# Kernel tuning notes

Measured on AMD Instinct MI355X. Metric: run time of the kernel, lower is better.

Reference implementation:

```python
import jax, jax.numpy as jnp
import numpy as np

B, C, U, LEN, K = 32, 16, 16, 128, 4  # batch, channels, units, image side, cheb order
POWERS = K + 1


def _path_chebyshev(n, k):
    """Chebyshev polynomials T_0..T_k of the rescaled normalized Laplacian of an
    undirected path graph with n nodes. Returns [k+1, n, n] float32."""
    A = np.zeros((n, n), dtype=np.float64)
    A[np.arange(n - 1), np.arange(1, n)] = 1.0
    A = A + A.T
    d = A.sum(axis=1)
    dinv = 1.0 / np.sqrt(d)
    L = np.eye(n) - dinv[:, None] * A * dinv[None, :]   # normalized Laplacian
    Lt = L - np.eye(n)                                   # rescaled: 2L/lambda_max - I, lambda_max=2
    T = [np.eye(n), Lt]
    for _ in range(2, k + 1):
        T.append(2.0 * Lt @ T[-1] - T[-2])
    return np.stack(T[: k + 1]).astype(np.float32)


def setup_inputs() -> dict:
    key = jax.random.key(0)
    kx, kc = jax.random.split(key)
    x = jax.random.normal(kx, (B, C, LEN, LEN), dtype=jnp.float32)
    coefs = 0.001 * jax.random.normal(kc, (POWERS, POWERS, C, U), dtype=jnp.float32)
    cheb = jnp.asarray(_path_chebyshev(LEN, K))  # same graph for both axes
    return {"x": x, "coefs": coefs, "cheb1": cheb, "cheb2": cheb}


def reference(x, coefs, cheb1, cheb2):
    # out[b,u,p,q] = sum_{k1,k2,c,h,w} coefs[k1,k2,c,u] * cheb1[k1,h,p] * x[b,c,h,w] * cheb2[k2,w,q]
    t1 = jnp.einsum('bchw,khp->bkcpw', x, cheb1)        # apply cheb1 along H
    s = jnp.einsum('bkcpw,klcu->blupw', t1, coefs)      # contract k1 and channels
    out = jnp.einsum('blupw,lwq->bupq', s, cheb2)       # apply cheb2 along W, contract k2
    return out
```

## Files before the change

kernel.cpp:

```cpp
#include <hip/hip_runtime.h>
#include <hip/hip_bf16.h>

#define LEN 128
#define NB 32
#define NC 16
#define NU 16
#define NK 5
#define KC 80
#define KCP 96

typedef unsigned int uint32;
typedef unsigned short ushort16;
typedef __attribute__((ext_vector_type(8))) short bf16x8;
typedef __attribute__((ext_vector_type(4))) float f32x4;

#define MFMA(a, b, c) __builtin_amdgcn_mfma_f32_16x16x32_bf16(a, b, c, 0, 0, 0)

#define SIG(r) (((r) & 15) ^ (((r) >> 3) & 15))

static __device__ inline ushort16 f2bf(float f) {
    union { float f; uint32 u; } v; v.f = f;
    uint32 u = v.u;
    uint32 r = (u + 0x7fffu + ((u >> 16) & 1u)) >> 16;
    return (ushort16)r;
}
static __device__ inline uint32 pkbf(float a, float b) {
    return (uint32)f2bf(a) | ((uint32)f2bf(b) << 16);
}
static __device__ inline bf16x8 frag16(const void* p) {
    return *(const bf16x8*)p;
}

__global__ __launch_bounds__(256) void kprep(const float* __restrict__ x,
                                             const float* __restrict__ coefs,
                                             const float* __restrict__ cheb1,
                                             const float* __restrict__ cheb2,
                                             ushort16* __restrict__ xF,
                                             ushort16* __restrict__ cheb1F,
                                             ushort16* __restrict__ cheb2F,
                                             ushort16* __restrict__ coefF,
                                             ushort16* __restrict__ t1, int ident) {
    __shared__ __align__(16) uint32 Xs[128 * 64];
    const int blk = blockIdx.x, tid = threadIdx.x;
    if (blk < 512) {
        const int bc = blk;
        const float* xp = x + (size_t)bc * (LEN * LEN);
        {
            int w = tid & 127, hg = tid >> 7;
            #pragma unroll
            for (int uu = 0; uu < 8; ++uu) {
                int u = hg * 8 + uu;
                uint4 d;
                uint32* dp = (uint32*)&d;
                #pragma unroll
                for (int t = 0; t < 4; ++t) {
                    int h2 = u * 4 + t;
                    dp[t] = pkbf(xp[(2 * h2) * LEN + w], xp[(2 * h2 + 1) * LEN + w]);
                }
                *(uint4*)(Xs + w * 64 + ((u ^ SIG(w)) << 2)) = d;
            }
        }
        if (ident) {
            const int b = bc >> 4, c = bc & 15;
            int p = tid >> 1, half = tid & 1;
            const float4* src = (const float4*)(xp + p * LEN + half * 64);
            ushort16* dst = t1 + ((size_t)(b * LEN + p) * KC + c) * LEN + half * 64;
            #pragma unroll
            for (int i = 0; i < 16; ++i) {
                float4 v = src[i];
                uint2 d;
                d.x = pkbf(v.x, v.y);
                d.y = pkbf(v.z, v.w);
                *(uint2*)(dst + i * 4) = d;
            }
        }
        __syncthreads();
        ushort16* dst = xF + (size_t)bc * 16384;
        #pragma unroll
        for (int i = 0; i < 8; ++i) {
            int n = tid + i * 256;
            int lane = n & 63, fk = n >> 6;
            int wrow = (fk >> 2) * 16 + (lane & 15);
            int u = (fk & 3) * 4 + (lane >> 4);
            uint4 v = *(const uint4*)(Xs + wrow * 64 + ((u ^ SIG(wrow)) << 2));
            *(uint4*)(dst + (size_t)n * 8) = v;
        }
    } else {
        int i = (blk - 512) * 256 + tid;
        if (i < 81920) {
            int j = i & 7, lane = (i >> 3) & 63, ks = (i >> 9) & 3, nt = i >> 11;
            int kp = nt * 16 + (lane & 15);
            int k = kp >> 7, p = kp & 127;
            int h = ks * 32 + ((lane >> 4) << 3) + j;
            cheb1F[i] = f2bf(cheb1[(k * LEN + h) * LEN + p]);
        } else if (i < 163840) {
            int i2 = i - 81920;
            int j = i2 & 7, lane = (i2 >> 3) & 63, t = i2 >> 9;
            int ks = t % 20, nt = t / 20;
            int q = nt * 16 + (lane & 15);
            int lw = ks * 32 + ((lane >> 4) << 3) + j;
            int l = lw >> 7, w = lw & 127;
            cheb2F[i2] = f2bf(cheb2[(l * LEN + w) * LEN + q]);
        } else {
            int i3 = i - 163840;
            int j = i3 & 7, lane = (i3 >> 3) & 63, t = i3 >> 9;
            int ks = t % 3, nt = t / 3;
            int lu = nt * 16 + (lane & 15);
            int l = lu >> 4, u = lu & 15;
            int kc = ks * 32 + ((lane >> 4) << 3) + j;
            int k = kc >> 4, c = kc & 15;
            coefF[i3] = (kc < KC) ? f2bf(coefs[((k * NK + l) * NC + c) * NU + u]) : (ushort16)0;
        }
    }
}

__global__ __launch_bounds__(256, 5) void k1_mfma(const ushort16* __restrict__ xF,
                                                  const ushort16* __restrict__ cheb1F,
                                                  const float* __restrict__ x,
                                                  ushort16* __restrict__ t1, int b0, int ident) {
    __shared__ __align__(16) uint32 Bs[64 * 64];
    const int c = blockIdx.x, bl = blockIdx.y, z = blockIdx.z;
    const int b = b0 + bl;
    const int tid = threadIdx.x;
    const int lane = tid & 63, wm = tid >> 6;
    const int m16 = lane & 15, g = lane >> 4;

    if (!ident && z == 0) {
        const float* xp = x + (size_t)(b * NC + c) * (LEN * LEN);
        int p = tid >> 1, half = tid & 1;
        const float4* src = (const float4*)(xp + p * LEN + half * 64);
        ushort16* dst = t1 + ((size_t)(bl * LEN + p) * KC + c) * LEN + half * 64;
        #pragma unroll
        for (int i = 0; i < 16; ++i) {
            float4 v = src[i];
            uint2 d;
            d.x = pkbf(v.x, v.y);
            d.y = pkbf(v.z, v.w);
            *(uint2*)(dst + i * 4) = d;
        }
    }

    const ushort16* xFb = xF + ((size_t)(b * NC + c)) * 16384;

    f32x4 acc[2][4];
    #pragma unroll
    for (int mi = 0; mi < 2; ++mi)
        #pragma unroll
        for (int ni = 0; ni < 4; ++ni) acc[mi][ni] = (f32x4)0.f;

    #pragma unroll
    for (int ks = 0; ks < 4; ++ks) {
        bf16x8 Af[2], Bf[4];
        #pragma unroll
        for (int mi = 0; mi < 2; ++mi) {
            int mt = wm * 2 + mi;
            Af[mi] = frag16(xFb + ((size_t)(mt * 4 + ks) * 64 + lane) * 8);
        }
        #pragma unroll
        for (int ni = 0; ni < 4; ++ni) {
            int nt = 8 + z * 4 + ni;
            Bf[ni] = frag16(cheb1F + ((size_t)(nt * 4 + ks) * 64 + lane) * 8);
        }
        #pragma unroll
        for (int mi = 0; mi < 2; ++mi)
            #pragma unroll
            for (int ni = 0; ni < 4; ++ni)
                acc[mi][ni] = MFMA(Af[mi], Bf[ni], acc[mi][ni]);
    }

    #pragma unroll
    for (int ni = 0; ni < 4; ++ni)
        #pragma unroll
        for (int mi = 0; mi < 2; ++mi) {
            int rr = ni * 16 + m16;
            int wu = wm * 32 + mi * 16 + g * 4;
            uint2 d;
            d.x = pkbf(acc[mi][ni][0], acc[mi][ni][1]);
            d.y = pkbf(acc[mi][ni][2], acc[mi][ni][3]);
            int u = wu >> 3;
            *(uint2*)(Bs + rr * 64 + ((u ^ SIG(rr)) << 2) + ((wu >> 1) & 3)) = d;
        }
    __syncthreads();

    #pragma unroll
    for (int i = 0; i < 4; ++i) {
        int n = tid + i * 256;
        int rr = n >> 4, wsg = n & 15;
        uint4 v = *(const uint4*)(Bs + rr * 64 + ((wsg ^ SIG(rr)) << 2));
        int kp = 128 + z * 64 + rr;
        int k = kp >> 7, p = kp & 127;
        *(uint4*)(t1 + ((size_t)((bl * LEN + p) * KC + k * NC + c)) * LEN + wsg * 8) = v;
    }
}

__global__ __launch_bounds__(256, 5) void k2_mfma(const ushort16* __restrict__ t1,
                                                  const ushort16* __restrict__ coefF,
                                                  const ushort16* __restrict__ cheb2F,
                                                  float* __restrict__ out, int b0) {
    __shared__ __align__(16) uint32 sm[128 * 64];
    const int p = blockIdx.x, bl = blockIdx.y, b = b0 + bl;
    const int tid = threadIdx.x;
    const int lane = tid & 63, wave = tid >> 6;
    const int n16 = lane & 15, g = lane >> 4;

    const uint32* t1u = (const uint32*)(t1 + (size_t)(bl * LEN + p) * (KC * LEN));
    uint4 Av[3], Bv[3];
    #pragma unroll
    for (int i = 0; i < 3; ++i) {
        int it = tid + i * 256;
        if (it < 640) {
            int a2 = it >> 4, wq = it & 15;
            const uint32* src = t1u + a2 * 128 + wq * 4;
            Av[i] = *(const uint4*)(src);
            Bv[i] = *(const uint4*)(src + 64);
        }
    }
    #pragma unroll
    for (int i = 0; i < 4; ++i) {
        int idx = tid + i * 256;
        int row = idx >> 3, d = idx & 7;
        int u = 10 + (d >> 2);
        sm[row * 64 + ((u ^ SIG(row)) << 2) + (d & 3)] = 0;
    }
    #pragma unroll
    for (int i = 0; i < 3; ++i) {
        int it = tid + i * 256;
        if (it < 640) {
            int a2 = it >> 4, wq = it & 15;
            const uint32* av = (const uint32*)&Av[i];
            const uint32* bv = (const uint32*)&Bv[i];
            int u = a2 >> 2, lo = a2 & 3;
            #pragma unroll
            for (int j = 0; j < 4; ++j) {
                int r0 = wq * 8 + 2 * j, r1 = r0 + 1;
                sm[r0 * 64 + ((u ^ SIG(r0)) << 2) + lo] = (av[j] & 0xffffu) | (bv[j] << 16);
                sm[r1 * 64 + ((u ^ SIG(r1)) << 2) + lo] = (av[j] >> 16) | (bv[j] & 0xffff0000u);
            }
        }
    }
    __syncthreads();

    f32x4 acc[2][5];
    #pragma unroll
    for (int mi = 0; mi < 2; ++mi)
        #pragma unroll
        for (int ni = 0; ni < 5; ++ni) acc[mi][ni] = (f32x4)0.f;

    #pragma unroll
    for (int ks = 0; ks < 3; ++ks) {
        bf16x8 Af[2], Bf[5];
        #pragma unroll
        for (int mi = 0; mi < 2; ++mi) {
            int row = wave * 32 + mi * 16 + n16;
            Af[mi] = frag16(sm + row * 64 + (((ks * 4 + g) ^ SIG(row)) << 2));
        }
        #pragma unroll
        for (int ni = 0; ni < 5; ++ni)
            Bf[ni] = frag16(coefF + ((size_t)(ni * 3 + ks) * 64 + lane) * 8);
        #pragma unroll
        for (int mi = 0; mi < 2; ++mi)
            #pragma unroll
            for (int ni = 0; ni < 5; ++ni)
                acc[mi][ni] = MFMA(Af[mi], Bf[ni], acc[mi][ni]);
    }
    __syncthreads();

    {
        ushort16* A3 = (ushort16*)sm;
        #pragma unroll
        for (int mi = 0; mi < 2; ++mi)
            #pragma unroll
            for (int ni = 0; ni < 5; ++ni) {
                int wcol = wave * 32 + mi * 16 + g * 4;
                uint2 d;
                d.x = pkbf(acc[mi][ni][0], acc[mi][ni][1]);
                d.y = pkbf(acc[mi][ni][2], acc[mi][ni][3]);
                *(uint2*)(A3 + n16 * 648 + ni * 128 + wcol) = d;
            }
    }
    __syncthreads();

    const ushort16* A3r = (const ushort16*)sm;
    f32x4 c3[2];
    c3[0] = (f32x4)0.f; c3[1] = (f32x4)0.f;
    #pragma unroll 4
    for (int ks = 4; ks < 20; ++ks) {
        bf16x8 Aa = frag16(A3r + n16 * 648 + ks * 32 + g * 8);
        #pragma unroll
        for (int nt = 0; nt < 2; ++nt) {
            bf16x8 Bb = frag16(cheb2F + ((size_t)((wave * 2 + nt) * 20 + ks) * 64 + lane) * 8);
            c3[nt] = MFMA(Aa, Bb, c3[nt]);
        }
    }

    #pragma unroll
    for (int nt = 0; nt < 2; ++nt)
        #pragma unroll
        for (int r = 0; r < 4; ++r) {
            int u = g * 4 + r;
            int q = wave * 32 + nt * 16 + n16;
            uint32 bf = ((uint32)A3r[u * 648 + q]) << 16;
            float l0 = __uint_as_float(bf);
            out[(((size_t)(b * NU + u)) * LEN + p) * LEN + q] = c3[nt][r] + l0;
        }
}

extern "C" void kernel_launch(void* const* d_in, const int* in_sizes, int n_in,
                              void* d_out, int out_size, void* d_ws, size_t ws_size,
                              hipStream_t stream) {
    const float* x     = (const float*)d_in[0];
    const float* coefs = (const float*)d_in[1];
    const float* cheb1 = (const float*)d_in[2];
    const float* cheb2 = (const float*)d_in[3];
    float* out = (float*)d_out;

    const size_t xF_bytes  = (size_t)NB * NC * 16384 * sizeof(ushort16);
    const size_t aux_bytes = 163840 + 163840 + 15360;
    size_t off = (ws_size - aux_bytes - xF_bytes) & ~(size_t)255;
    ushort16* cheb1F = (ushort16*)((char*)d_ws + off);
    ushort16* cheb2F = cheb1F + 81920;
    ushort16* coefF  = cheb2F + 81920;
    ushort16* xF     = coefF + 7680;
    ushort16* t1 = (ushort16*)d_ws;

    const size_t per_b = (size_t)LEN * KC * LEN * sizeof(ushort16);
    int chunk = (int)(off / per_b);
    if (chunk < 1) chunk = 1;
    if (chunk > NB) chunk = NB;
    const int ident = (chunk == NB) ? 1 : 0;

    hipLaunchKernelGGL(kprep, dim3(1182), dim3(256), 0, stream,
                       x, coefs, cheb1, cheb2, xF, cheb1F, cheb2F, coefF, t1, ident);
    for (int b0 = 0; b0 < NB; b0 += chunk) {
        int cb = (NB - b0 < chunk) ? (NB - b0) : chunk;
        hipLaunchKernelGGL(k1_mfma, dim3(NC, cb, 8), dim3(256), 0, stream,
                           xF, cheb1F, x, t1, b0, ident);
        hipLaunchKernelGGL(k2_mfma, dim3(LEN, cb), dim3(256), 0, stream,
                           t1, coefF, cheb2F, out, b0);
    }
}
```

Baseline: 154.0 us.

## Process four rows per k2 block, keep cheb2 fragments in registers, prefetch next row

The k2 kernel now handles four p-rows per block instead of one, and the grid shrinks from 128 to 32 blocks per batch. The cheb2 B-fragments are loaded into registers once per block and reused across the four rows instead of being re-read from global memory each time. While the current row is computed, the next row's t1 data is loaded into registers. This raises register pressure (launch bounds lowered from 5 to 4 waves) and reduces the number of blocks available to hide latency.

```diff
diff --git a/kernel.cpp b/kernel.cpp
--- a/kernel.cpp
+++ b/kernel.cpp
@@ -193,116 +193,142 @@
     }
 }
 
-__global__ __launch_bounds__(256, 5) void k2_mfma(const ushort16* __restrict__ t1,
+__global__ __launch_bounds__(256, 4) void k2_mfma(const ushort16* __restrict__ t1,
                                                   const ushort16* __restrict__ coefF,
                                                   const ushort16* __restrict__ cheb2F,
                                                   float* __restrict__ out, int b0) {
     __shared__ __align__(16) uint32 sm[128 * 64];
-    const int p = blockIdx.x, bl = blockIdx.y, b = b0 + bl;
+    const int pblk = blockIdx.x, bl = blockIdx.y, b = b0 + bl;
     const int tid = threadIdx.x;
     const int lane = tid & 63, wave = tid >> 6;
     const int n16 = lane & 15, g = lane >> 4;
 
-    const uint32* t1u = (const uint32*)(t1 + (size_t)(bl * LEN + p) * (KC * LEN));
+    bf16x8 B3[32];
+    #pragma unroll
+    for (int nt = 0; nt < 2; ++nt)
+        #pragma unroll
+        for (int ks = 4; ks < 20; ++ks)
+            B3[nt * 16 + ks - 4] =
+                frag16(cheb2F + ((size_t)((wave * 2 + nt) * 20 + ks) * 64 + lane) * 8);
+
+    const uint32* t1base = (const uint32*)(t1 + (size_t)(bl * LEN + pblk * 4) * (KC * LEN));
+
     uint4 Av[3], Bv[3];
     #pragma unroll
     for (int i = 0; i < 3; ++i) {
         int it = tid + i * 256;
         if (it < 640) {
             int a2 = it >> 4, wq = it & 15;
-            const uint32* src = t1u + a2 * 128 + wq * 4;
+            const uint32* src = t1base + a2 * 128 + wq * 4;
             Av[i] = *(const uint4*)(src);
             Bv[i] = *(const uint4*)(src + 64);
         }
     }
-    #pragma unroll
-    for (int i = 0; i < 4; ++i) {
-        int idx = tid + i * 256;
-        int row = idx >> 3, d = idx & 7;
-        int u = 10 + (d >> 2);
-        sm[row * 64 + ((u ^ SIG(row)) << 2) + (d & 3)] = 0;
-    }
-    #pragma unroll
-    for (int i = 0; i < 3; ++i) {
-        int it = tid + i * 256;
-        if (it < 640) {
-            int a2 = it >> 4, wq = it & 15;
-            const uint32* av = (const uint32*)&Av[i];
-            const uint32* bv = (const uint32*)&Bv[i];
-            int u = a2 >> 2, lo = a2 & 3;
-            #pragma unroll
-            for (int j = 0; j < 4; ++j) {
-                int r0 = wq * 8 + 2 * j, r1 = r0 + 1;
-                sm[r0 * 64 + ((u ^ SIG(r0)) << 2) + lo] = (av[j] & 0xffffu) | (bv[j] << 16);
-                sm[r1 * 64 + ((u ^ SIG(r1)) << 2) + lo] = (av[j] >> 16) | (bv[j] & 0xffff0000u);
-            }
-        }
-    }
-    __syncthreads();
-
-    f32x4 acc[2][5];
-    #pragma unroll
-    for (int mi = 0; mi < 2; ++mi)
-        #pragma unroll
-        for (int ni = 0; ni < 5; ++ni) acc[mi][ni] = (f32x4)0.f;
-
-    #pragma unroll
-    for (int ks = 0; ks < 3; ++ks) {
-        bf16x8 Af[2], Bf[5];
-        #pragma unroll
-        for (int mi = 0; mi < 2; ++mi) {
-            int row = wave * 32 + mi * 16 + n16;
-            Af[mi] = frag16(sm + row * 64 + (((ks * 4 + g) ^ SIG(row)) << 2));
-        }
-        #pragma unroll
-        for (int ni = 0; ni < 5; ++ni)
-            Bf[ni] = frag16(coefF + ((size_t)(ni * 3 + ks) * 64 + lane) * 8);
+
+    for (int pi = 0; pi < 4; ++pi) {
+        const int p = pblk * 4 + pi;
+        if (pi) __syncthreads();
+
+        #pragma unroll
+        for (int i = 0; i < 4; ++i) {
+            int idx = tid + i * 256;
+            int row = idx >> 3, d = idx & 7;
+            int u = 10 + (d >> 2);
+            sm[row * 64 + ((u ^ SIG(row)) << 2) + (d & 3)] = 0;
+        }
+        #pragma unroll
+        for (int i = 0; i < 3; ++i) {
+            int it = tid + i * 256;
+            if (it < 640) {
+                int a2 = it >> 4, wq = it & 15;
+                const uint32* av = (const uint32*)&Av[i];
+                const uint32* bv = (const uint32*)&Bv[i];
+                int u = a2 >> 2, lo = a2 & 3;
+                #pragma unroll
+                for (int j = 0; j < 4; ++j) {
+                    int r0 = wq * 8 + 2 * j, r1 = r0 + 1;
+                    sm[r0 * 64 + ((u ^ SIG(r0)) << 2) + lo] = (av[j] & 0xffffu) | (bv[j] << 16);
+                    sm[r1 * 64 + ((u ^ SIG(r1)) << 2) + lo] = (av[j] >> 16) | (bv[j] & 0xffff0000u);
+                }
+            }
+        }
+        __syncthreads();
+
+        if (pi < 3) {
+            const uint32* nsrc = t1base + (size_t)(pi + 1) * 5120;
+            #pragma unroll
+            for (int i = 0; i < 3; ++i) {
+                int it = tid + i * 256;
+                if (it < 640) {
+                    int a2 = it >> 4, wq = it & 15;
+                    const uint32* src = nsrc + a2 * 128 + wq * 4;
+                    Av[i] = *(const uint4*)(src);
+                    Bv[i] = *(const uint4*)(src + 64);
+                }
+            }
+        }
+
+        f32x4 acc[2][5];
         #pragma unroll
         for (int mi = 0; mi < 2; ++mi)
             #pragma unroll
+            for (int ni = 0; ni < 5; ++ni) acc[mi][ni] = (f32x4)0.f;
+
+        #pragma unroll
+        for (int ks = 0; ks < 3; ++ks) {
+            bf16x8 Af[2], Bf[5];
+            #pragma unroll
+            for (int mi = 0; mi < 2; ++mi) {
+                int row = wave * 32 + mi * 16 + n16;
+                Af[mi] = frag16(sm + row * 64 + (((ks * 4 + g) ^ SIG(row)) << 2));
+            }
+            #pragma unroll
             for (int ni = 0; ni < 5; ++ni)
-                acc[mi][ni] = MFMA(Af[mi], Bf[ni], acc[mi][ni]);
-    }
-    __syncthreads();
-
-    {
-        ushort16* A3 = (ushort16*)sm;
-        #pragma unroll
-        for (int mi = 0; mi < 2; ++mi)
-            #pragma unroll
-            for (int ni = 0; ni < 5; ++ni) {
-                int wcol = wave * 32 + mi * 16 + g * 4;
-                uint2 d;
-                d.x = pkbf(acc[mi][ni][0], acc[mi][ni][1]);
-                d.y = pkbf(acc[mi][ni][2], acc[mi][ni][3]);
-                *(uint2*)(A3 + n16 * 648 + ni * 128 + wcol) = d;
-            }
-    }
-    __syncthreads();
-
-    const ushort16* A3r = (const ushort16*)sm;
-    f32x4 c3[2];
-    c3[0] = (f32x4)0.f; c3[1] = (f32x4)0.f;
-    #pragma unroll 4
-    for (int ks = 4; ks < 20; ++ks) {
-        bf16x8 Aa = frag16(A3r + n16 * 648 + ks * 32 + g * 8);
-        #pragma unroll
-        for (int nt = 0; nt < 2; ++nt) {
-            bf16x8 Bb = frag16(cheb2F + ((size_t)((wave * 2 + nt) * 20 + ks) * 64 + lane) * 8);
-            c3[nt] = MFMA(Aa, Bb, c3[nt]);
-        }
-    }
-
-    #pragma unroll
-    for (int nt = 0; nt < 2; ++nt)
-        #pragma unroll
-        for (int r = 0; r < 4; ++r) {
-            int u = g * 4 + r;
-            int q = wave * 32 + nt * 16 + n16;
-            uint32 bf = ((uint32)A3r[u * 648 + q]) << 16;
-            float l0 = __uint_as_float(bf);
-            out[(((size_t)(b * NU + u)) * LEN + p) * LEN + q] = c3[nt][r] + l0;
-        }
+                Bf[ni] = frag16(coefF + ((size_t)(ni * 3 + ks) * 64 + lane) * 8);
+            #pragma unroll
+            for (int mi = 0; mi < 2; ++mi)
+                #pragma unroll
+                for (int ni = 0; ni < 5; ++ni)
+                    acc[mi][ni] = MFMA(Af[mi], Bf[ni], acc[mi][ni]);
+        }
+        __syncthreads();
+
+        {
+            ushort16* A3 = (ushort16*)sm;
+            #pragma unroll
+            for (int mi = 0; mi < 2; ++mi)
+                #pragma unroll
+                for (int ni = 0; ni < 5; ++ni) {
+                    int wcol = wave * 32 + mi * 16 + g * 4;
+                    uint2 d;
+                    d.x = pkbf(acc[mi][ni][0], acc[mi][ni][1]);
+                    d.y = pkbf(acc[mi][ni][2], acc[mi][ni][3]);
+                    *(uint2*)(A3 + n16 * 648 + ni * 128 + wcol) = d;
+                }
+        }
+        __syncthreads();
+
+        const ushort16* A3r = (const ushort16*)sm;
+        f32x4 c3[2];
+        c3[0] = (f32x4)0.f; c3[1] = (f32x4)0.f;
+        #pragma unroll
+        for (int ks = 4; ks < 20; ++ks) {
+            bf16x8 Aa = frag16(A3r + n16 * 648 + ks * 32 + g * 8);
+            c3[0] = MFMA(Aa, B3[ks - 4], c3[0]);
+            c3[1] = MFMA(Aa, B3[16 + ks - 4], c3[1]);
+        }
+
+        #pragma unroll
+        for (int nt = 0; nt < 2; ++nt)
+            #pragma unroll
+            for (int r = 0; r < 4; ++r) {
+                int u = g * 4 + r;
+                int q = wave * 32 + nt * 16 + n16;
+                uint32 bf = ((uint32)A3r[u * 648 + q]) << 16;
+                float l0 = __uint_as_float(bf);
+                out[(((size_t)(b * NU + u)) * LEN + p) * LEN + q] = c3[nt][r] + l0;
+            }
+    }
 }
 
 extern "C" void kernel_launch(void* const* d_in, const int* in_sizes, int n_in,
@@ -335,7 +361,7 @@
         int cb = (NB - b0 < chunk) ? (NB - b0) : chunk;
         hipLaunchKernelGGL(k1_mfma, dim3(NC, cb, 8), dim3(256), 0, stream,
                            xF, cheb1F, x, t1, b0, ident);
-        hipLaunchKernelGGL(k2_mfma, dim3(LEN, cb), dim3(256), 0, stream,
+        hipLaunchKernelGGL(k2_mfma, dim3(32, cb), dim3(256), 0, stream,
                            t1, coefF, cheb2F, out, b0);
     }
 }
```

Result: slower. 355.3 us (+130.8%).
